# Kernel tuning notes

Hardware: AMD Instinct MI355X
Metric: run time of the kernel (lower is better)

The kernel has to match this reference:

```python
import jax, jax.numpy as jnp
import numpy as np

B, T, N, C = 8, 16, 2048, 512


def setup_inputs() -> dict:
    key = jax.random.key(0)
    k1, k2, k3, k4, k5, k6 = jax.random.split(key, 6)
    return {
        "vd_s": jax.random.normal(k1, (B, T, C), dtype=jnp.float32),
        "vd_nodes": jax.random.normal(k2, (B, N, C), dtype=jnp.float32),
        # 1x1 conv weights initialized N(0, 0.01) as in the torch module
        "W1": jax.random.normal(k3, (C, C), dtype=jnp.float32) * 0.01,
        "b1": jax.random.normal(k4, (C,), dtype=jnp.float32) * 0.01,
        "W2": jax.random.normal(k5, (C, C), dtype=jnp.float32) * 0.01,
        "b2": jax.random.normal(k6, (C,), dtype=jnp.float32) * 0.01,
    }


def reference(vd_s, vd_nodes, W1, b1, W2, b2):
    # propagation_step = 1 (as in the original module)
    def per_graph(s, nodes):
        # s: [T, C] scene features, nodes: [N, C] node features
        out_scene = s.mean(axis=0)                     # [C]
        state = nodes                                  # [N, C]
        # 1x1 convs on [N, C, 1, 1] == per-node linear layers
        mat1 = state @ W1.T + b1                       # [N, C]
        mat2 = state @ W2.T + b2                       # [N, C]
        adj = mat1 @ mat2.T                            # [N, N]
        soft_adj = jax.nn.softmax(adj, axis=1)         # row-softmax (dim=1)
        new_state = soft_adj @ state + state           # message update + residual
        gp_out = new_state.mean(axis=0)                # [C]
        return jnp.concatenate([out_scene, gp_out], axis=0)  # [2C]

    return jax.vmap(per_graph)(vd_s, vd_nodes)         # [B, 2C]
```

## Files before the change

kernel.cpp:

```cpp
#include <hip/hip_runtime.h>

typedef __bf16 bf16;
typedef __bf16 bf16x8 __attribute__((ext_vector_type(8), aligned(16)));
typedef float  f32x4  __attribute__((ext_vector_type(4)));
typedef float  f32x2  __attribute__((ext_vector_type(2)));

#define B_ 8
#define T_ 16
#define N_ 2048
#define C_ 512

__device__ inline bf16x8 load8_f32(const float* p) {
    float4 a = *(const float4*)p;
    float4 b = *(const float4*)(p + 4);
    bf16x8 r;
    r[0] = (bf16)a.x; r[1] = (bf16)a.y; r[2] = (bf16)a.z; r[3] = (bf16)a.w;
    r[4] = (bf16)b.x; r[5] = (bf16)b.y; r[6] = (bf16)b.z; r[7] = (bf16)b.w;
    return r;
}

__device__ inline void gload_lds16(const void* g, void* l) {
    __builtin_amdgcn_global_load_lds(
        (const __attribute__((address_space(1))) void*)g,
        (__attribute__((address_space(3))) void*)l, 16, 0, 0);
}

__device__ inline unsigned char f32_to_fp8(float v) {
    int p = __builtin_amdgcn_cvt_pk_fp8_f32(v, 0.f, 0, false);
    return (unsigned char)(p & 0xff);
}

__device__ inline void fp8x4_to_f32(unsigned int wd, float* o) {
    f32x2 lo = __builtin_amdgcn_cvt_pk_f32_fp8((int)wd, false);
    f32x2 hi = __builtin_amdgcn_cvt_pk_f32_fp8((int)wd, true);
    o[0] = lo[0]; o[1] = lo[1]; o[2] = hi[0]; o[3] = hi[1];
}

__global__ __launch_bounds__(256) void k_prep(
    const float* __restrict__ vd_s, const float* __restrict__ nodes,
    const float* __restrict__ W1, const float* __restrict__ W2,
    float* __restrict__ out, bf16* __restrict__ nodes_bf,
    unsigned char* __restrict__ nodes_f8,
    bf16* __restrict__ W1t, bf16* __restrict__ W2t) {
    __shared__ float sh[32 * 33];
    const int bx = blockIdx.x, tid = threadIdx.x;
    if (bx < 2048) {
        size_t i = ((size_t)bx * 256 + tid) * 16;
        float v[16];
        *(float4*)&v[0]  = *(const float4*)(nodes + i);
        *(float4*)&v[4]  = *(const float4*)(nodes + i + 4);
        *(float4*)&v[8]  = *(const float4*)(nodes + i + 8);
        *(float4*)&v[12] = *(const float4*)(nodes + i + 12);
        bf16x8 b0, b1;
#pragma unroll
        for (int e = 0; e < 8; ++e) { b0[e] = (bf16)v[e]; b1[e] = (bf16)v[8 + e]; }
        *(bf16x8*)(nodes_bf + i)     = b0;
        *(bf16x8*)(nodes_bf + i + 8) = b1;
        uint4 u;
        unsigned int wds[4];
#pragma unroll
        for (int k = 0; k < 4; ++k) {
            int p = __builtin_amdgcn_cvt_pk_fp8_f32(v[k * 4 + 0], v[k * 4 + 1], 0, false);
            p = __builtin_amdgcn_cvt_pk_fp8_f32(v[k * 4 + 2], v[k * 4 + 3], p, true);
            wds[k] = (unsigned int)p;
        }
        u.x = wds[0]; u.y = wds[1]; u.z = wds[2]; u.w = wds[3];
        *(uint4*)(nodes_f8 + i) = u;
    } else if (bx < 2064) {
        int gt = (bx - 2048) * 256 + tid;
        int b = gt >> 9, c = gt & 511;
        float s = 0.f;
#pragma unroll
        for (int t = 0; t < T_; ++t) s += vd_s[(size_t)b * T_ * C_ + t * C_ + c];
        out[b * 2 * C_ + c] = s * (1.0f / T_);
    } else {
        const float* W = (bx < 2320) ? W1 : W2;
        bf16* Wt = (bx < 2320) ? W1t : W2t;
        int idx = (bx < 2320) ? bx - 2064 : bx - 2320;
        int bxx = (idx & 15) * 32, byy = (idx >> 4) * 32;
        int tx = tid & 31, ty = tid >> 5;
#pragma unroll
        for (int r = 0; r < 32; r += 8)
            sh[(ty + r) * 33 + tx] = W[(size_t)(byy + ty + r) * C_ + bxx + tx];
        __syncthreads();
#pragma unroll
        for (int r = 0; r < 32; r += 8)
            Wt[(size_t)(bxx + ty + r) * C_ + byy + tx] = (bf16)sh[tx * 33 + ty + r];
    }
}

__global__ void k_q(const float* __restrict__ b1, const bf16* __restrict__ W2t,
                    float* __restrict__ q) {
    int wid = threadIdx.x >> 6, lane = threadIdx.x & 63;
    int c = blockIdx.x * 4 + wid;
    bf16x8 v8 = *(const bf16x8*)(W2t + (size_t)c * C_ + lane * 8);
    float s = 0.f;
#pragma unroll
    for (int i = 0; i < 8; ++i) s += (float)v8[i] * b1[lane * 8 + i];
#pragma unroll
    for (int m = 32; m; m >>= 1) s += __shfl_xor(s, m);
    if (lane == 0) q[c] = s;
}

template <int OM>
__global__ __launch_bounds__(256) void gemm_nt(
    const bf16* __restrict__ A, size_t strideA,
    const bf16* __restrict__ Bm, size_t strideB,
    const float* __restrict__ bias,
    void* __restrict__ Cv, size_t strideC,
    int N, int K) {
    __shared__ __attribute__((aligned(16))) bf16 lA[128 * 64];
    __shared__ __attribute__((aligned(16))) bf16 lB[128 * 64];
    const int tid = threadIdx.x;
    const int lane = tid & 63, w = tid >> 6;
    const int wm = w >> 1, wn = w & 1;
    const int z = blockIdx.z;
    const int bm = blockIdx.x * 128, bn = blockIdx.y * 128;
    const bf16* Ab = A + (size_t)z * strideA;
    const bf16* Bb = Bm + (size_t)z * strideB;

    f32x4 acc[4][4];
#pragma unroll
    for (int i = 0; i < 4; ++i)
#pragma unroll
        for (int j = 0; j < 4; ++j) acc[i][j] = f32x4{0.f, 0.f, 0.f, 0.f};

    const int nkt = K >> 6;
    for (int kt = 0; kt < nkt; ++kt) {
#pragma unroll
        for (int c = 0; c < 4; ++c) {
            int ca = c * 256 + tid;
            int row = ca >> 3;
            int qd = (ca & 7) ^ (row & 7);
            gload_lds16(Ab + (size_t)(bm + row) * K + kt * 64 + qd * 8,
                        lA + c * 2048 + w * 512);
            gload_lds16(Bb + (size_t)(bn + row) * K + kt * 64 + qd * 8,
                        lB + c * 2048 + w * 512);
        }
        __syncthreads();

        bf16x8 af[2][4], bfr[2][4];
#pragma unroll
        for (int ks = 0; ks < 2; ++ks) {
            int y = ks * 4 + (lane >> 4);
#pragma unroll
            for (int i = 0; i < 4; ++i) {
                int ra = wm * 64 + i * 16 + (lane & 15);
                int rb = wn * 64 + i * 16 + (lane & 15);
                af[ks][i]  = *(const bf16x8*)&lA[ra * 64 + ((y ^ (ra & 7)) * 8)];
                bfr[ks][i] = *(const bf16x8*)&lB[rb * 64 + ((y ^ (rb & 7)) * 8)];
            }
        }
#pragma unroll
        for (int ks = 0; ks < 2; ++ks)
#pragma unroll
            for (int i = 0; i < 4; ++i)
#pragma unroll
                for (int j = 0; j < 4; ++j)
                    acc[i][j] = __builtin_amdgcn_mfma_f32_16x16x32_bf16(
                        af[ks][i], bfr[ks][j], acc[i][j], 0, 0, 0);
        __syncthreads();
    }

#pragma unroll
    for (int i = 0; i < 4; ++i) {
#pragma unroll
        for (int j = 0; j < 4; ++j) {
            int col = bn + wn * 64 + j * 16 + (lane & 15);
            float bv = bias ? bias[col] : 0.f;
#pragma unroll
            for (int r = 0; r < 4; ++r) {
                int row = bm + wm * 64 + i * 16 + (lane >> 4) * 4 + r;
                float v = acc[i][j][r] + bv;
                if constexpr (OM == 0) {
                    ((bf16*)Cv)[(size_t)z * strideC + (size_t)row * N + col] = (bf16)v;
                } else {
                    ((unsigned char*)Cv)[(size_t)z * strideC + (size_t)row * N + col] =
                        f32_to_fp8(v * 16.0f);
                }
            }
        }
    }
}

__global__ __launch_bounds__(512, 2) void gemm256p(
    const unsigned char* __restrict__ A, const unsigned char* __restrict__ Bm,
    unsigned char* __restrict__ P) {
    __shared__ __attribute__((aligned(16))) unsigned char ls[2][2][16384];
    const int tid = threadIdx.x;
    const int lane = tid & 63, w = tid >> 6;
    const int wm = w >> 2, wn = w & 3;
    const int qh = lane >> 5, ql = (lane >> 4) & 1;
    const int id = blockIdx.x;
    const int sw = (id & 7) * 64 + (id >> 3);
    const int z = sw >> 6, tt = sw & 63;
    const int bm = (tt >> 3) * 256, bn = (tt & 7) * 256;
    const unsigned char* Ab = A + (size_t)z * N_ * C_;
    const unsigned char* Bb = Bm + (size_t)z * N_ * C_;

    f32x4 acc[8][4];
#pragma unroll
    for (int i = 0; i < 8; ++i)
#pragma unroll
        for (int j = 0; j < 4; ++j) acc[i][j] = f32x4{0.f, 0.f, 0.f, 0.f};

#define STAGE_T(kt_, buf_)                                                        \
    {                                                                             \
        _Pragma("unroll")                                                         \
        for (int l = 0; l < 2; ++l) {                                             \
            int ca = l * 512 + tid;                                               \
            int row = ca >> 2;                                                    \
            int qd = (ca & 3) ^ ((row >> 1) & 3);                                 \
            gload_lds16(Ab + (size_t)(bm + row) * 512 + (kt_) * 64 + qd * 16,     \
                        &ls[buf_][0][(l * 512 + w * 64) * 16]);                   \
            gload_lds16(Bb + (size_t)(bn + row) * 512 + (kt_) * 64 + qd * 16,     \
                        &ls[buf_][1][(l * 512 + w * 64) * 16]);                   \
        }                                                                         \
    }

    STAGE_T(0, 0);
    STAGE_T(1, 1);
    asm volatile("s_waitcnt vmcnt(4)" ::: "memory");
    __builtin_amdgcn_s_barrier();
    asm volatile("" ::: "memory");

#pragma unroll
    for (int j = 0; j < 8; ++j) {
        const int cur = j & 1;
        const unsigned char* lA = &ls[cur][0][0];
        const unsigned char* lB = &ls[cur][1][0];

        long af[8][2], bfv[4][2];
#pragma unroll
        for (int i = 0; i < 8; ++i) {
            int ra = wm * 128 + i * 16 + (lane & 15);
            int rr = (ra >> 1) & 3;
#pragma unroll
            for (int ks = 0; ks < 2; ++ks)
                af[i][ks] = *(const long*)&lA[ra * 64 + (((ks * 2 + qh) ^ rr) * 16) + ql * 8];
        }
#pragma unroll
        for (int jj = 0; jj < 4; ++jj) {
            int rb = wn * 64 + jj * 16 + (lane & 15);
            int rr = (rb >> 1) & 3;
#pragma unroll
            for (int ks = 0; ks < 2; ++ks)
                bfv[jj][ks] = *(const long*)&lB[rb * 64 + (((ks * 2 + qh) ^ rr) * 16) + ql * 8];
        }
        __builtin_amdgcn_s_setprio(1);
#pragma unroll
        for (int ks = 0; ks < 2; ++ks)
#pragma unroll
            for (int i = 0; i < 8; ++i)
#pragma unroll
                for (int jj = 0; jj < 4; ++jj)
                    acc[i][jj] = __builtin_amdgcn_mfma_f32_16x16x32_fp8_fp8(
                        af[i][ks], bfv[jj][ks], acc[i][jj], 0, 0, 0);
        __builtin_amdgcn_s_setprio(0);

        asm volatile("" ::: "memory");
        __builtin_amdgcn_s_barrier();
        asm volatile("" ::: "memory");

        if (j + 2 < 8) STAGE_T(j + 2, cur);
        if (j < 7) {
            if (j < 6) asm volatile("s_waitcnt vmcnt(4)" ::: "memory");
            else       asm volatile("s_waitcnt vmcnt(0)" ::: "memory");
            __builtin_amdgcn_s_barrier();
            asm volatile("" ::: "memory");
        }
    }

    unsigned char* Pb = P + (size_t)z * N_ * N_;
#pragma unroll
    for (int fi = 0; fi < 8; ++fi) {
#pragma unroll
        for (int fj = 0; fj < 4; ++fj) {
            int roff = (fi >> 2) * 64 + (fi & 3) * 16;
            int coff = (fj >> 1) * 32 + (fj & 1) * 16;
            int col = bn + wn * 64 + coff + (lane & 15);
#pragma unroll
            for (int r = 0; r < 4; ++r) {
                int row = bm + wm * 128 + roff + (lane >> 4) * 4 + r;
                float v = __expf(fminf(acc[fi][fj][r] * 0.0625f, 8.8f)) * 0.0625f;
                Pb[(size_t)row * N_ + col] = f32_to_fp8(v);
            }
        }
    }
#undef STAGE_T
}

__global__ __launch_bounds__(256) void k_w2(const unsigned char* __restrict__ P,
                                            float* __restrict__ wpart) {
    __shared__ float rp[16 * 256];
    __shared__ float ri[16];
    const int tid = threadIdx.x;
    const int s = blockIdx.x, b = blockIdx.y;
    const unsigned char* Pb = P + (size_t)b * N_ * N_ + (size_t)s * 16 * N_;
    const int j0 = tid * 8;
    uint2 v[16];
#pragma unroll
    for (int r = 0; r < 16; ++r) {
        v[r] = *(const uint2*)&Pb[(size_t)r * N_ + j0];
        float f[8];
        fp8x4_to_f32(v[r].x, &f[0]);
        fp8x4_to_f32(v[r].y, &f[4]);
        float t = 0.f;
#pragma unroll
        for (int e = 0; e < 8; ++e) t += f[e];
        rp[r * 256 + tid] = t;
    }
    __syncthreads();
    {
        int row = tid >> 4, seg = tid & 15;
        float t = 0.f;
#pragma unroll
        for (int k = 0; k < 16; ++k) t += rp[row * 256 + seg + 16 * k];
#pragma unroll
        for (int m = 8; m; m >>= 1) t += __shfl_xor(t, m);
        if (seg == 0) ri[row] = 1.0f / t;
    }
    __syncthreads();
    float acc8[8] = {0.f, 0.f, 0.f, 0.f, 0.f, 0.f, 0.f, 0.f};
#pragma unroll
    for (int r = 0; r < 16; ++r) {
        float rr = ri[r];
        float f[8];
        fp8x4_to_f32(v[r].x, &f[0]);
        fp8x4_to_f32(v[r].y, &f[4]);
#pragma unroll
        for (int e = 0; e < 8; ++e) acc8[e] += rr * f[e];
    }
    float* wp = wpart + ((size_t)b * 128 + s) * (size_t)N_;
#pragma unroll
    for (int e = 0; e < 8; ++e) wp[j0 + e] = acc8[e];
}

__global__ __launch_bounds__(256) void k_gp(const bf16* __restrict__ nodes_bf,
                                            const float* __restrict__ wpart,
                                            float* __restrict__ gppart) {
    __shared__ float wred[4][64];
    __shared__ float wsh[64];
    __shared__ float gred[4][512];
    const int tid = threadIdx.x;
    const int slab = blockIdx.x, b = blockIdx.y;
    const int jj = tid & 63, sg = tid >> 6;
    float wacc = 0.f;
    for (int s = sg; s < 128; s += 4)
        wacc += wpart[((size_t)b * 128 + s) * N_ + slab * 64 + jj];
    wred[sg][jj] = wacc;
    __syncthreads();
    if (tid < 64)
        wsh[tid] = wred[0][tid] + wred[1][tid] + wred[2][tid] + wred[3][tid] + 1.0f;
    __syncthreads();
    const int j0 = slab * 64;
    const int cc = (tid & 63) * 8, jr = tid >> 6;
    const bf16* nb = nodes_bf + (size_t)b * N_ * C_;
    float acc8[8] = {0.f, 0.f, 0.f, 0.f, 0.f, 0.f, 0.f, 0.f};
    for (int j = jr; j < 64; j += 4) {
        float wj = wsh[j];
        bf16x8 nv = *(const bf16x8*)&nb[(size_t)(j0 + j) * C_ + cc];
#pragma unroll
        for (int e = 0; e < 8; ++e) acc8[e] += wj * (float)nv[e];
    }
#pragma unroll
    for (int e = 0; e < 8; ++e) gred[jr][cc + e] = acc8[e];
    __syncthreads();
    if (tid < 64) {
#pragma unroll
        for (int e = 0; e < 8; ++e) {
            int c = tid * 8 + e;
            gppart[((size_t)slab * 8 + b) * C_ + c] =
                gred[0][c] + gred[1][c] + gred[2][c] + gred[3][c];
        }
    }
}

__global__ void k_fin(const float* __restrict__ gppart, float* __restrict__ out) {
    int gt = blockIdx.x * 256 + threadIdx.x;
    int b = gt >> 9, c = gt & 511;
    float s = 0.f;
#pragma unroll
    for (int k = 0; k < 32; ++k) s += gppart[((size_t)k * 8 + b) * C_ + c];
    out[b * 2 * C_ + C_ + c] = s * (1.0f / N_);
}

extern "C" void kernel_launch(void* const* d_in, const int* in_sizes, int n_in,
                              void* d_out, int out_size, void* d_ws, size_t ws_size,
                              hipStream_t stream) {
    const float* vd_s  = (const float*)d_in[0];
    const float* nodes = (const float*)d_in[1];
    const float* W1    = (const float*)d_in[2];
    const float* b1    = (const float*)d_in[3];
    const float* W2    = (const float*)d_in[4];
    float* out = (float*)d_out;

    char* ws = (char*)d_ws;
    bf16*          nodes_bf = (bf16*)(ws);
    unsigned char* H2f8     = (unsigned char*)(ws + ((size_t)16 << 20));
    float*         wpart    = (float*)(ws + ((size_t)16 << 20));
    unsigned char* nodes_f8 = (unsigned char*)(ws + ((size_t)24 << 20));
    unsigned char* P        = (unsigned char*)(ws + ((size_t)32 << 20));
    bf16*          W1t      = (bf16*)(ws + ((size_t)96 << 20));
    bf16*          W2t      = (bf16*)(ws + ((size_t)96 << 20) + (512u << 10));
    bf16*          Gt       = (bf16*)(ws + ((size_t)96 << 20) + (1024u << 10));
    char*          fbase    = ws + ((size_t)96 << 20) + (1536u << 10);
    float*         q        = (float*)(fbase);
    float*         gppart   = (float*)(fbase + 4096);

    k_prep<<<2576, 256, 0, stream>>>(vd_s, nodes, W1, W2,
                                     out, nodes_bf, nodes_f8, W1t, W2t);
    k_q<<<128, 256, 0, stream>>>(b1, W2t, q);

    gemm_nt<0><<<dim3(4, 4, 1), 256, 0, stream>>>(
        W2t, 0, W1t, 0, nullptr, Gt, 0, C_, C_);
    gemm_nt<1><<<dim3(16, 4, 8), 256, 0, stream>>>(
        nodes_bf, (size_t)N_ * C_, Gt, 0, q,
        H2f8, (size_t)N_ * C_, C_, C_);
    gemm256p<<<512, 512, 0, stream>>>(H2f8, nodes_f8, P);

    k_w2<<<dim3(128, 8), 256, 0, stream>>>(P, wpart);
    k_gp<<<dim3(32, 8), 256, 0, stream>>>(nodes_bf, wpart, gppart);
    k_fin<<<16, 256, 0, stream>>>(gppart, out);
}
```

Before: 110.8 us.

## Split fp8 logits GEMM across 16 waves and read fp8 nodes in k_gp

The fused fp8 adjacency-GEMM-plus-exp kernel now runs 1024 threads per 256x256 tile instead of 512. Each wave owns a 64x64 sub-tile, so accumulators and fragments are halved and each thread issues one async load per operand per stage, with the vmcnt waits adjusted to match. The aim is more latency hiding per tile at the cost of more LDS fragment traffic and higher barrier cost per block. Separately, k_gp now reads node features in fp8 instead of bf16, halving its memory traffic but lowering the precision of the weighted node sum.

```diff
diff --git a/kernel.cpp b/kernel.cpp
--- a/kernel.cpp
+++ b/kernel.cpp
@@ -183,7 +183,7 @@
     }
 }
 
-__global__ __launch_bounds__(512, 2) void gemm256p(
+__global__ __launch_bounds__(1024, 4) void gemm256w(
     const unsigned char* __restrict__ A, const unsigned char* __restrict__ Bm,
     unsigned char* __restrict__ P) {
     __shared__ __attribute__((aligned(16))) unsigned char ls[2][2][16384];
@@ -198,29 +198,25 @@
     const unsigned char* Ab = A + (size_t)z * N_ * C_;
     const unsigned char* Bb = Bm + (size_t)z * N_ * C_;
 
-    f32x4 acc[8][4];
-#pragma unroll
-    for (int i = 0; i < 8; ++i)
+    f32x4 acc[4][4];
+#pragma unroll
+    for (int i = 0; i < 4; ++i)
 #pragma unroll
         for (int j = 0; j < 4; ++j) acc[i][j] = f32x4{0.f, 0.f, 0.f, 0.f};
 
 #define STAGE_T(kt_, buf_)                                                        \
     {                                                                             \
-        _Pragma("unroll")                                                         \
-        for (int l = 0; l < 2; ++l) {                                             \
-            int ca = l * 512 + tid;                                               \
-            int row = ca >> 2;                                                    \
-            int qd = (ca & 3) ^ ((row >> 1) & 3);                                 \
-            gload_lds16(Ab + (size_t)(bm + row) * 512 + (kt_) * 64 + qd * 16,     \
-                        &ls[buf_][0][(l * 512 + w * 64) * 16]);                   \
-            gload_lds16(Bb + (size_t)(bn + row) * 512 + (kt_) * 64 + qd * 16,     \
-                        &ls[buf_][1][(l * 512 + w * 64) * 16]);                   \
-        }                                                                         \
+        int row = tid >> 2;                                                       \
+        int qd = (tid & 3) ^ ((row >> 1) & 3);                                    \
+        gload_lds16(Ab + (size_t)(bm + row) * 512 + (kt_) * 64 + qd * 16,         \
+                    &ls[buf_][0][w * 1024]);                                      \
+        gload_lds16(Bb + (size_t)(bn + row) * 512 + (kt_) * 64 + qd * 16,         \
+                    &ls[buf_][1][w * 1024]);                                      \
     }
 
     STAGE_T(0, 0);
     STAGE_T(1, 1);
-    asm volatile("s_waitcnt vmcnt(4)" ::: "memory");
+    asm volatile("s_waitcnt vmcnt(2)" ::: "memory");
     __builtin_amdgcn_s_barrier();
     asm volatile("" ::: "memory");
 
@@ -230,10 +226,10 @@
         const unsigned char* lA = &ls[cur][0][0];
         const unsigned char* lB = &ls[cur][1][0];
 
-        long af[8][2], bfv[4][2];
-#pragma unroll
-        for (int i = 0; i < 8; ++i) {
-            int ra = wm * 128 + i * 16 + (lane & 15);
+        long af[4][2], bfv[4][2];
+#pragma unroll
+        for (int i = 0; i < 4; ++i) {
+            int ra = wm * 64 + i * 16 + (lane & 15);
             int rr = (ra >> 1) & 3;
 #pragma unroll
             for (int ks = 0; ks < 2; ++ks)
@@ -251,7 +247,7 @@
 #pragma unroll
         for (int ks = 0; ks < 2; ++ks)
 #pragma unroll
-            for (int i = 0; i < 8; ++i)
+            for (int i = 0; i < 4; ++i)
 #pragma unroll
                 for (int jj = 0; jj < 4; ++jj)
                     acc[i][jj] = __builtin_amdgcn_mfma_f32_16x16x32_fp8_fp8(
@@ -264,7 +260,7 @@
 
         if (j + 2 < 8) STAGE_T(j + 2, cur);
         if (j < 7) {
-            if (j < 6) asm volatile("s_waitcnt vmcnt(4)" ::: "memory");
+            if (j < 6) asm volatile("s_waitcnt vmcnt(2)" ::: "memory");
             else       asm volatile("s_waitcnt vmcnt(0)" ::: "memory");
             __builtin_amdgcn_s_barrier();
             asm volatile("" ::: "memory");
@@ -273,15 +269,13 @@
 
     unsigned char* Pb = P + (size_t)z * N_ * N_;
 #pragma unroll
-    for (int fi = 0; fi < 8; ++fi) {
+    for (int fi = 0; fi < 4; ++fi) {
 #pragma unroll
         for (int fj = 0; fj < 4; ++fj) {
-            int roff = (fi >> 2) * 64 + (fi & 3) * 16;
-            int coff = (fj >> 1) * 32 + (fj & 1) * 16;
-            int col = bn + wn * 64 + coff + (lane & 15);
+            int col = bn + wn * 64 + fj * 16 + (lane & 15);
 #pragma unroll
             for (int r = 0; r < 4; ++r) {
-                int row = bm + wm * 128 + roff + (lane >> 4) * 4 + r;
+                int row = bm + wm * 64 + fi * 16 + (lane >> 4) * 4 + r;
                 float v = __expf(fminf(acc[fi][fj][r] * 0.0625f, 8.8f)) * 0.0625f;
                 Pb[(size_t)row * N_ + col] = f32_to_fp8(v);
             }
@@ -336,7 +330,7 @@
     for (int e = 0; e < 8; ++e) wp[j0 + e] = acc8[e];
 }
 
-__global__ __launch_bounds__(256) void k_gp(const bf16* __restrict__ nodes_bf,
+__global__ __launch_bounds__(256) void k_gp(const unsigned char* __restrict__ nodes_f8,
                                             const float* __restrict__ wpart,
                                             float* __restrict__ gppart) {
     __shared__ float wred[4][64];
@@ -355,13 +349,16 @@
     __syncthreads();
     const int j0 = slab * 64;
     const int cc = (tid & 63) * 8, jr = tid >> 6;
-    const bf16* nb = nodes_bf + (size_t)b * N_ * C_;
+    const unsigned char* nb = nodes_f8 + (size_t)b * N_ * C_;
     float acc8[8] = {0.f, 0.f, 0.f, 0.f, 0.f, 0.f, 0.f, 0.f};
     for (int j = jr; j < 64; j += 4) {
         float wj = wsh[j];
-        bf16x8 nv = *(const bf16x8*)&nb[(size_t)(j0 + j) * C_ + cc];
-#pragma unroll
-        for (int e = 0; e < 8; ++e) acc8[e] += wj * (float)nv[e];
+        uint2 nv = *(const uint2*)&nb[(size_t)(j0 + j) * C_ + cc];
+        float f[8];
+        fp8x4_to_f32(nv.x, &f[0]);
+        fp8x4_to_f32(nv.y, &f[4]);
+#pragma unroll
+        for (int e = 0; e < 8; ++e) acc8[e] += wj * f[e];
     }
 #pragma unroll
     for (int e = 0; e < 8; ++e) gred[jr][cc + e] = acc8[e];
@@ -417,9 +414,9 @@
     gemm_nt<1><<<dim3(16, 4, 8), 256, 0, stream>>>(
         nodes_bf, (size_t)N_ * C_, Gt, 0, q,
         H2f8, (size_t)N_ * C_, C_, C_);
-    gemm256p<<<512, 512, 0, stream>>>(H2f8, nodes_f8, P);
+    gemm256w<<<512, 1024, 0, stream>>>(H2f8, nodes_f8, P);
 
     k_w2<<<dim3(128, 8), 256, 0, stream>>>(P, wpart);
-    k_gp<<<dim3(32, 8), 256, 0, stream>>>(nodes_bf, wpart, gppart);
+    k_gp<<<dim3(32, 8), 256, 0, stream>>>(nodes_f8, wpart, gppart);
     k_fin<<<16, 256, 0, stream>>>(gppart, out);
 }
```

After: 108.6 us. 2.0% less time.
